# Performance work log

Hardware: AMD Instinct MI355X
Metric: run time of the kernel (lower is better)

## Reference

```python
import jax, jax.numpy as jnp
import numpy as np

C = 256
G = 32            # GroupNorm groups = min(32, C)
DQK = C // 8      # q/k channel dim
EPS = 1e-5


def setup_inputs() -> dict:
    key = jax.random.key(0)
    ks = jax.random.split(key, 10)
    B, H, W = 4, 64, 64
    s = 0.02
    return {
        "x": jax.random.normal(ks[0], (B, C, H, W), dtype=jnp.float32),
        "gamma": jnp.ones((C,), jnp.float32),
        "beta": jnp.zeros((C,), jnp.float32),
        "wq": jax.random.normal(ks[1], (DQK, C), jnp.float32) * s,
        "bq": jnp.zeros((DQK,), jnp.float32),
        "wk": jax.random.normal(ks[2], (DQK, C), jnp.float32) * s,
        "bk": jnp.zeros((DQK,), jnp.float32),
        "wv": jax.random.normal(ks[3], (C, C), jnp.float32) * s,
        "bv": jnp.zeros((C,), jnp.float32),
        "wp": jax.random.normal(ks[4], (C, C), jnp.float32) * s,
        "bp": jnpp if False else jnp.zeros((C,), jnp.float32),
    }


def reference(x, gamma, beta, wq, bq, wk, bk, wv, bv, wp, bp):
    B, Cc, H, W = x.shape
    N = H * W
    # GroupNorm(32, C), affine
    h = x.reshape(B, G, Cc // G, H, W)
    mu = h.mean(axis=(2, 3, 4), keepdims=True)
    var = h.var(axis=(2, 3, 4), keepdims=True)
    h = (h - mu) * jax.lax.rsqrt(var + EPS)
    h = h.reshape(B, Cc, N) * gamma[:, None] + beta[:, None]
    # 1x1 convs == per-token linear maps over channels
    q = jnp.einsum('dc,bcn->bnd', wq, h) + bq            # [B, N, DQK]
    k = jnp.einsum('dc,bcn->bdn', wk, h) + bk[:, None]   # [B, DQK, N]
    v = jnp.einsum('ec,bcn->ben', wv, h) + bv[:, None]   # [B, C, N]
    scale = DQK ** (-0.5)
    attn = jax.nn.softmax(jnp.einsum('bnd,bdm->bnm', q, k) * scale, axis=-1)
    out = jnp.einsum('bnm,bem->ben', attn, v)            # [B, C, N]
    proj = jnp.einsum('fe,ben->bfn', wp, out) + bp[:, None]
    return x + proj.reshape(B, Cc, H, W)
```

## Files before the change

### kernel.cpp

```cpp
#include <hip/hip_runtime.h>
#include <hip/hip_bf16.h>

#define NB 4
#define CD 256
#define NT 4096
#define DQ 32

typedef __attribute__((ext_vector_type(8))) __bf16 bf16x8;
typedef __attribute__((ext_vector_type(4))) float float4v;
typedef __attribute__((ext_vector_type(16))) float float16v;
typedef __attribute__((ext_vector_type(4))) unsigned int uint4v;
typedef __attribute__((ext_vector_type(2))) unsigned int uint2v;

#if __has_builtin(__builtin_amdgcn_exp2f)
#define EXP2(x) __builtin_amdgcn_exp2f(x)
#else
#define EXP2(x) exp2f(x)
#endif

__device__ inline unsigned short f2bf(float f) {
  unsigned u = __float_as_uint(f);
  u += 0x7fffu + ((u >> 16) & 1u);
  return (unsigned short)(u >> 16);
}

__global__ __launch_bounds__(256) void gn_prep(
    const float* __restrict__ x, float* __restrict__ accum,
    const float* __restrict__ wq, const float* __restrict__ wk,
    const float* __restrict__ wv, const float* __restrict__ wp,
    const float* __restrict__ bq, const float* __restrict__ bk,
    const float* __restrict__ bv, unsigned short* __restrict__ wqkv,
    unsigned short* __restrict__ wpb, float* __restrict__ bias) {
  int bx = blockIdx.x;
  int tid = threadIdx.x;
  if (bx < 512) {
    int bg = bx >> 2, ch = bx & 3;
    const float4* xp = (const float4*)(x + (size_t)bg * 32768 + ch * 8192);
    float s = 0.f, ss = 0.f;
#pragma unroll
    for (int i = 0; i < 8; i++) {
      float4 v = xp[tid + 256 * i];
      s += v.x + v.y + v.z + v.w;
      ss += v.x * v.x + v.y * v.y + v.z * v.z + v.w * v.w;
    }
    int wid = tid >> 6, lane = tid & 63;
#pragma unroll
    for (int off = 32; off >= 1; off >>= 1) {
      s += __shfl_xor(s, off);
      ss += __shfl_xor(ss, off);
    }
    __shared__ float red[8];
    if (lane == 0) { red[wid] = s; red[4 + wid] = ss; }
    __syncthreads();
    if (tid == 0) {
      accum[2 * bx] = red[0] + red[1] + red[2] + red[3];
      accum[2 * bx + 1] = red[4] + red[5] + red[6] + red[7];
    }
  } else {
    const float scale2 = 0.2550348909867343f;
    int i = (bx - 512) * 256 + tid;
    if (i < 320 * 256) {
      int j = i >> 8, c = i & 255;
      float v;
      if (j < 32) v = wq[j * 256 + c] * scale2;
      else if (j < 64) v = wk[(j - 32) * 256 + c];
      else v = wv[(j - 64) * 256 + c];
      wqkv[i] = f2bf(v);
    } else if (i < 320 * 256 + 256 * 256) {
      int k = i - 320 * 256;
      wpb[k] = f2bf(wp[k]);
    } else if (i < 320 * 256 + 256 * 256 + 320) {
      int j = i - (320 * 256 + 256 * 256);
      float v;
      if (j < 32) v = bq[j] * scale2;
      else if (j < 64) v = bk[j - 32];
      else v = bv[j - 64];
      bias[j] = v;
    }
  }
}

__global__ __launch_bounds__(256) void gn_apply(
    const float* __restrict__ x, const float* __restrict__ gamma,
    const float* __restrict__ beta, const float* __restrict__ accum,
    unsigned short* __restrict__ h) {
  int bg = blockIdx.x >> 2, nc = blockIdx.x & 3;
  int tid = threadIdx.x;
  float S = accum[8 * bg] + accum[8 * bg + 2] + accum[8 * bg + 4] +
            accum[8 * bg + 6];
  float SS = accum[8 * bg + 1] + accum[8 * bg + 3] + accum[8 * bg + 5] +
             accum[8 * bg + 7];
  float mu = S * (1.f / 32768.f);
  float var = SS * (1.f / 32768.f) - mu * mu;
  float rstd = rsqrtf(var + 1e-5f);
  int b = bg >> 5, g = bg & 31, c0 = g * 8;
  float gam[8], bet[8];
#pragma unroll
  for (int j = 0; j < 8; j++) { gam[j] = gamma[c0 + j]; bet[j] = beta[c0 + j]; }
  const float* xb = x + (size_t)bg * 32768;
#pragma unroll
  for (int i = 0; i < 4; i++) {
    int n = nc * 1024 + tid + 256 * i;
    unsigned short hv[8];
#pragma unroll
    for (int j = 0; j < 8; j++) {
      float y = (xb[j * NT + n] - mu) * rstd * gam[j] + bet[j];
      hv[j] = f2bf(y);
    }
    *(uint4v*)(h + ((size_t)(b * NT + n) * CD + c0)) = *(uint4v*)hv;
  }
}

__global__ __launch_bounds__(256) void qkv_gemm(
    const unsigned short* __restrict__ A, const unsigned short* __restrict__ H,
    const float* __restrict__ bias, unsigned short* __restrict__ qk,
    unsigned short* __restrict__ v) {
  int nt = blockIdx.x, mt = blockIdx.y, b = blockIdx.z;
  int tid = threadIdx.x, lane = tid & 63;
  int w = tid >> 6, mi = w & 1, ni = w >> 1;
  int l31 = lane & 31, hh = lane >> 5;
  int m_base = mt * 64 + 32 * mi;
  int n_base = nt * 128 + 64 * ni;
  const unsigned short* Arow = A + (size_t)(m_base + l31) * 256 + 8 * hh;
  const unsigned short* Hb = H + (size_t)b * NT * CD;
  const unsigned short* h0 = Hb + (size_t)(n_base + l31) * CD + 8 * hh;
  const unsigned short* h1 = h0 + (size_t)32 * CD;
  float16v acc0, acc1;
#pragma unroll
  for (int r = 0; r < 16; r++) { acc0[r] = 0.f; acc1[r] = 0.f; }
#pragma unroll
  for (int s = 0; s < 16; s++) {
    bf16x8 af = *(const bf16x8*)(Arow + 16 * s);
    bf16x8 b0 = *(const bf16x8*)(h0 + 16 * s);
    bf16x8 b1 = *(const bf16x8*)(h1 + 16 * s);
    acc0 = __builtin_amdgcn_mfma_f32_32x32x16_bf16(af, b0, acc0, 0, 0, 0);
    acc1 = __builtin_amdgcn_mfma_f32_32x32x16_bf16(af, b1, acc1, 0, 0, 0);
  }
  float bj[16];
  int jr[16];
#pragma unroll
  for (int r = 0; r < 16; r++) {
    jr[r] = m_base + (r & 3) + 8 * (r >> 2) + 4 * hh;
    bj[r] = bias[jr[r]];
  }
#pragma unroll
  for (int half = 0; half < 2; half++) {
    int n = n_base + 32 * half + l31;
#pragma unroll
    for (int r = 0; r < 16; r++) {
      float val = (half ? acc1[r] : acc0[r]) + bj[r];
      int j = jr[r];
      if (j < 64) {
        qk[((size_t)b * NT + n) * 64 + j] = f2bf(val);
      } else {
        v[((size_t)b * CD + (j - 64)) * NT + n] = f2bf(val);
      }
    }
  }
}

__global__ __launch_bounds__(256) void attn_fused(
    const unsigned short* __restrict__ qk, const unsigned short* __restrict__ V,
    unsigned short* __restrict__ Pa, unsigned short* __restrict__ Pb,
    float* __restrict__ lp4) {
  int bx = blockIdx.x;
  int n0 = (bx >> 1) * 64;
  int kh = bx & 1;
  int E0 = blockIdx.y * 128;
  int b = blockIdx.z;
  int tid = threadIdx.x, lane = tid & 63, w = tid >> 6;
  int qi = w & 1, ei = w >> 1;
  int l31 = lane & 31, hh = lane >> 5;

  __shared__ unsigned short Ks[64 * 36];
  __shared__ unsigned short Vs[128 * 68];
  __shared__ unsigned short Pbuf[2 * 32 * 68];

  const unsigned short* qkb = qk + (size_t)b * NT * 64;
  const unsigned short* Vb = V + (size_t)b * CD * NT;

  int n_g = n0 + 32 * qi + l31;
  bf16x8 qfr[2];
  qfr[0] = *(const bf16x8*)&qkb[(size_t)n_g * 64 + 8 * hh];
  qfr[1] = *(const bf16x8*)&qkb[(size_t)n_g * 64 + 8 * hh + 16];

  int se = tid >> 1, smh = (tid & 1) * 32;
  int skr = tid >> 2, skc = (tid & 3) * 8;

  int mbase = kh * 2048;
  uint4v vreg[4];
  uint4v kreg;
  {
    const unsigned short* vp = &Vb[(size_t)(E0 + se) * NT + mbase + smh];
#pragma unroll
    for (int u = 0; u < 4; u++) vreg[u] = *(const uint4v*)(vp + 8 * u);
    kreg = *(const uint4v*)&qkb[(size_t)(mbase + skr) * 64 + 32 + skc];
  }

  float16v acc[2];
#pragma unroll
  for (int et = 0; et < 2; et++)
#pragma unroll
    for (int r = 0; r < 16; r++) acc[et][r] = 0.f;
  float lsum = 0.f;
  unsigned short* Prow = &Pbuf[(qi * 32 + l31) * 68];

  for (int it = 0; it < 32; it++) {
    *(uint4v*)&Ks[skr * 36 + skc] = kreg;
    if (it + 1 < 32) {
      int m1 = mbase + (it + 1) * 64;
      kreg = *(const uint4v*)&qkb[(size_t)(m1 + skr) * 64 + 32 + skc];
    }
    __syncthreads();

#pragma unroll
    for (int u = 0; u < 4; u++)
      *(uint4v*)&Vs[se * 68 + smh + 8 * u] = vreg[u];
    if (it + 1 < 32) {
      int m1 = mbase + (it + 1) * 64;
      const unsigned short* vp = &Vb[(size_t)(E0 + se) * NT + m1 + smh];
#pragma unroll
      for (int u = 0; u < 4; u++) vreg[u] = *(const uint4v*)(vp + 8 * u);
    }

    float16v st;
#pragma unroll
    for (int r = 0; r < 16; r++) st[r] = 0.f;
#pragma unroll
    for (int s = 0; s < 2; s++) {
      bf16x8 af = *(const bf16x8*)&Ks[(32 * ei + l31) * 36 + 16 * s + 8 * hh];
      st = __builtin_amdgcn_mfma_f32_32x32x16_bf16(af, qfr[s], st, 0, 0, 0);
    }
#pragma unroll
    for (int rq = 0; rq < 4; rq++) {
      float e0 = EXP2(st[4 * rq + 0]);
      float e1 = EXP2(st[4 * rq + 1]);
      float e2 = EXP2(st[4 * rq + 2]);
      float e3 = EXP2(st[4 * rq + 3]);
      lsum += (e0 + e1) + (e2 + e3);
      uint2v pw;
      pw[0] = __builtin_amdgcn_perm(__float_as_uint(e1), __float_as_uint(e0),
                                    0x07060302u);
      pw[1] = __builtin_amdgcn_perm(__float_as_uint(e3), __float_as_uint(e2),
                                    0x07060302u);
      *(uint2v*)&Prow[8 * rq + 4 * hh + 32 * ei] = pw;
    }
    __syncthreads();

#pragma unroll
    for (int sp = 0; sp < 4; sp++) {
      bf16x8 afr =
          *(const bf16x8*)&Pbuf[(qi * 32 + l31) * 68 + 16 * sp + 8 * hh];
#pragma unroll
      for (int et = 0; et < 2; et++) {
        bf16x8 bfr = *(const bf16x8*)&Vs[(64 * ei + 32 * et + l31) * 68 +
                                         16 * sp + 8 * hh];
        acc[et] =
            __builtin_amdgcn_mfma_f32_32x32x16_bf16(afr, bfr, acc[et], 0, 0, 0);
      }
    }
  }

  lsum += __shfl_xor(lsum, 32);
  unsigned short* Pout = (kh ? Pb : Pa) + (size_t)b * NT * CD;
#pragma unroll
  for (int r = 0; r < 16; r++) {
    int nl = (r & 3) + 8 * (r >> 2) + 4 * hh;
    size_t row = (size_t)(n0 + 32 * qi + nl) * CD + E0 + 64 * ei + l31;
#pragma unroll
    for (int et = 0; et < 2; et++) {
      Pout[row + 32 * et] = f2bf(acc[et][r]);
    }
  }
  if (hh == 0) {
    lp4[(size_t)((kh * 2 + ei) * NB + b) * NT + n0 + 32 * qi + l31] = lsum;
  }
}

__device__ inline bf16x8 combine_frag(const unsigned short* p0,
                                      const unsigned short* p1, float inv) {
  uint4v ua = *(const uint4v*)p0;
  uint4v ub = *(const uint4v*)p1;
  uint4v r;
#pragma unroll
  for (int j = 0; j < 4; j++) {
    float lo = __uint_as_float(ua[j] << 16) + __uint_as_float(ub[j] << 16);
    float hi = __uint_as_float(ua[j] & 0xffff0000u) +
               __uint_as_float(ub[j] & 0xffff0000u);
    lo *= inv;
    hi *= inv;
    r[j] = __builtin_amdgcn_perm(__float_as_uint(hi), __float_as_uint(lo),
                                 0x07060302u);
  }
  return *(bf16x8*)&r;
}

__global__ __launch_bounds__(256) void proj_gemm(
    const unsigned short* __restrict__ Wp, const unsigned short* __restrict__ Pa,
    const unsigned short* __restrict__ Pb, const float* __restrict__ lp4,
    const float* __restrict__ bp, const float* __restrict__ x,
    float* __restrict__ out) {
  int nt = blockIdx.x, mt = blockIdx.y, b = blockIdx.z;
  int tid = threadIdx.x, lane = tid & 63;
  int w = tid >> 6, mi = w & 1, ni = w >> 1;
  int l31 = lane & 31, hh = lane >> 5;
  int m_base = mt * 64 + 32 * mi;
  int n_base = nt * 128 + 64 * ni;
  const unsigned short* Arow = Wp + (size_t)(m_base + l31) * 256 + 8 * hh;
  int nA = n_base + l31, nB = nA + 32;
  float lA = 0.f, lB = 0.f;
#pragma unroll
  for (int s4 = 0; s4 < 4; s4++) {
    lA += lp4[(size_t)(s4 * NB + b) * NT + nA];
    lB += lp4[(size_t)(s4 * NB + b) * NT + nB];
  }
  float invA = 1.f / lA, invB = 1.f / lB;
  const unsigned short* a0 = Pa + ((size_t)b * NT + nA) * CD + 8 * hh;
  const unsigned short* a1 = Pa + ((size_t)b * NT + nB) * CD + 8 * hh;
  const unsigned short* c0 = Pb + ((size_t)b * NT + nA) * CD + 8 * hh;
  const unsigned short* c1 = Pb + ((size_t)b * NT + nB) * CD + 8 * hh;
  float16v acc0, acc1;
#pragma unroll
  for (int r = 0; r < 16; r++) { acc0[r] = 0.f; acc1[r] = 0.f; }
#pragma unroll
  for (int s = 0; s < 16; s++) {
    bf16x8 af = *(const bf16x8*)(Arow + 16 * s);
    bf16x8 b0 = combine_frag(a0 + 16 * s, c0 + 16 * s, invA);
    bf16x8 b1 = combine_frag(a1 + 16 * s, c1 + 16 * s, invB);
    acc0 = __builtin_amdgcn_mfma_f32_32x32x16_bf16(af, b0, acc0, 0, 0, 0);
    acc1 = __builtin_amdgcn_mfma_f32_32x32x16_bf16(af, b1, acc1, 0, 0, 0);
  }
#pragma unroll
  for (int half = 0; half < 2; half++) {
    int n = n_base + 32 * half + l31;
#pragma unroll
    for (int r = 0; r < 16; r++) {
      int f = m_base + (r & 3) + 8 * (r >> 2) + 4 * hh;
      size_t idx = ((size_t)b * CD + f) * NT + n;
      out[idx] = x[idx] + (half ? acc1[r] : acc0[r]) + bp[f];
    }
  }
}

extern "C" void kernel_launch(void* const* d_in, const int* in_sizes, int n_in,
                              void* d_out, int out_size, void* d_ws,
                              size_t ws_size, hipStream_t stream) {
  (void)in_sizes; (void)n_in; (void)out_size; (void)ws_size;
  const float* x = (const float*)d_in[0];
  const float* gamma = (const float*)d_in[1];
  const float* beta = (const float*)d_in[2];
  const float* wq = (const float*)d_in[3];
  const float* bq = (const float*)d_in[4];
  const float* wk = (const float*)d_in[5];
  const float* bk = (const float*)d_in[6];
  const float* wv = (const float*)d_in[7];
  const float* bv = (const float*)d_in[8];
  const float* wp = (const float*)d_in[9];
  const float* bp = (const float*)d_in[10];
  float* out = (float*)d_out;

  char* ws = (char*)d_ws;
  unsigned short* h_ws = (unsigned short*)ws;
  unsigned short* qk_ws = (unsigned short*)(ws + 8388608);
  unsigned short* v_ws = (unsigned short*)(ws + 10485760);
  unsigned short* o_ws = (unsigned short*)(ws + 18874368);
  unsigned short* wqkv_b = (unsigned short*)(ws + 27262976);
  unsigned short* wp_b = (unsigned short*)(ws + 27426816);
  float* bias_q = (float*)(ws + 27557888);
  float* accum = (float*)(ws + 27559168);
  float* lp4 = (float*)(ws + 27563264);

  gn_prep<<<1090, 256, 0, stream>>>(x, accum, wq, wk, wv, wp, bq, bk, bv,
                                    wqkv_b, wp_b, bias_q);
  gn_apply<<<512, 256, 0, stream>>>(x, gamma, beta, accum, h_ws);
  dim3 gq(32, 5, NB);
  qkv_gemm<<<gq, 256, 0, stream>>>(wqkv_b, h_ws, bias_q, qk_ws, v_ws);
  dim3 ga(128, 2, NB);
  attn_fused<<<ga, 256, 0, stream>>>(qk_ws, v_ws, h_ws, o_ws, lp4);
  dim3 gp(32, 4, NB);
  proj_gemm<<<gp, 256, 0, stream>>>(wp_b, h_ws, o_ws, lp4, bp, x, out);
}
```

Before: 207.9 us.

## Merge five kernels into one cooperative persistent kernel with grid syncs

Replaces the five separate launches (stats/weight prep, groupnorm apply, QKV GEMM, attention, projection) with a single cooperative kernel of 512 persistent blocks. The blocks loop over each stage's work items and separate the stages with grid-wide barriers. The aim is to remove per-launch overhead and the gaps between kernels. In exchange, the stages with 640 and 1024 work items no longer divide evenly across 512 blocks, grid syncs have their own cost, and occupancy is capped by the launch bounds and shared-memory use.

```diff
diff --git a/kernel.cpp b/kernel.cpp
--- a/kernel.cpp
+++ b/kernel.cpp
@@ -1,13 +1,15 @@
 #include <hip/hip_runtime.h>
 #include <hip/hip_bf16.h>
+#include <hip/hip_cooperative_groups.h>
 
 #define NB 4
 #define CD 256
 #define NT 4096
 #define DQ 32
 
+namespace cg = cooperative_groups;
+
 typedef __attribute__((ext_vector_type(8))) __bf16 bf16x8;
-typedef __attribute__((ext_vector_type(4))) float float4v;
 typedef __attribute__((ext_vector_type(16))) float float16v;
 typedef __attribute__((ext_vector_type(4))) unsigned int uint4v;
 typedef __attribute__((ext_vector_type(2))) unsigned int uint2v;
@@ -22,259 +24,6 @@
   unsigned u = __float_as_uint(f);
   u += 0x7fffu + ((u >> 16) & 1u);
   return (unsigned short)(u >> 16);
-}
-
-__global__ __launch_bounds__(256) void gn_prep(
-    const float* __restrict__ x, float* __restrict__ accum,
-    const float* __restrict__ wq, const float* __restrict__ wk,
-    const float* __restrict__ wv, const float* __restrict__ wp,
-    const float* __restrict__ bq, const float* __restrict__ bk,
-    const float* __restrict__ bv, unsigned short* __restrict__ wqkv,
-    unsigned short* __restrict__ wpb, float* __restrict__ bias) {
-  int bx = blockIdx.x;
-  int tid = threadIdx.x;
-  if (bx < 512) {
-    int bg = bx >> 2, ch = bx & 3;
-    const float4* xp = (const float4*)(x + (size_t)bg * 32768 + ch * 8192);
-    float s = 0.f, ss = 0.f;
-#pragma unroll
-    for (int i = 0; i < 8; i++) {
-      float4 v = xp[tid + 256 * i];
-      s += v.x + v.y + v.z + v.w;
-      ss += v.x * v.x + v.y * v.y + v.z * v.z + v.w * v.w;
-    }
-    int wid = tid >> 6, lane = tid & 63;
-#pragma unroll
-    for (int off = 32; off >= 1; off >>= 1) {
-      s += __shfl_xor(s, off);
-      ss += __shfl_xor(ss, off);
-    }
-    __shared__ float red[8];
-    if (lane == 0) { red[wid] = s; red[4 + wid] = ss; }
-    __syncthreads();
-    if (tid == 0) {
-      accum[2 * bx] = red[0] + red[1] + red[2] + red[3];
-      accum[2 * bx + 1] = red[4] + red[5] + red[6] + red[7];
-    }
-  } else {
-    const float scale2 = 0.2550348909867343f;
-    int i = (bx - 512) * 256 + tid;
-    if (i < 320 * 256) {
-      int j = i >> 8, c = i & 255;
-      float v;
-      if (j < 32) v = wq[j * 256 + c] * scale2;
-      else if (j < 64) v = wk[(j - 32) * 256 + c];
-      else v = wv[(j - 64) * 256 + c];
-      wqkv[i] = f2bf(v);
-    } else if (i < 320 * 256 + 256 * 256) {
-      int k = i - 320 * 256;
-      wpb[k] = f2bf(wp[k]);
-    } else if (i < 320 * 256 + 256 * 256 + 320) {
-      int j = i - (320 * 256 + 256 * 256);
-      float v;
-      if (j < 32) v = bq[j] * scale2;
-      else if (j < 64) v = bk[j - 32];
-      else v = bv[j - 64];
-      bias[j] = v;
-    }
-  }
-}
-
-__global__ __launch_bounds__(256) void gn_apply(
-    const float* __restrict__ x, const float* __restrict__ gamma,
-    const float* __restrict__ beta, const float* __restrict__ accum,
-    unsigned short* __restrict__ h) {
-  int bg = blockIdx.x >> 2, nc = blockIdx.x & 3;
-  int tid = threadIdx.x;
-  float S = accum[8 * bg] + accum[8 * bg + 2] + accum[8 * bg + 4] +
-            accum[8 * bg + 6];
-  float SS = accum[8 * bg + 1] + accum[8 * bg + 3] + accum[8 * bg + 5] +
-             accum[8 * bg + 7];
-  float mu = S * (1.f / 32768.f);
-  float var = SS * (1.f / 32768.f) - mu * mu;
-  float rstd = rsqrtf(var + 1e-5f);
-  int b = bg >> 5, g = bg & 31, c0 = g * 8;
-  float gam[8], bet[8];
-#pragma unroll
-  for (int j = 0; j < 8; j++) { gam[j] = gamma[c0 + j]; bet[j] = beta[c0 + j]; }
-  const float* xb = x + (size_t)bg * 32768;
-#pragma unroll
-  for (int i = 0; i < 4; i++) {
-    int n = nc * 1024 + tid + 256 * i;
-    unsigned short hv[8];
-#pragma unroll
-    for (int j = 0; j < 8; j++) {
-      float y = (xb[j * NT + n] - mu) * rstd * gam[j] + bet[j];
-      hv[j] = f2bf(y);
-    }
-    *(uint4v*)(h + ((size_t)(b * NT + n) * CD + c0)) = *(uint4v*)hv;
-  }
-}
-
-__global__ __launch_bounds__(256) void qkv_gemm(
-    const unsigned short* __restrict__ A, const unsigned short* __restrict__ H,
-    const float* __restrict__ bias, unsigned short* __restrict__ qk,
-    unsigned short* __restrict__ v) {
-  int nt = blockIdx.x, mt = blockIdx.y, b = blockIdx.z;
-  int tid = threadIdx.x, lane = tid & 63;
-  int w = tid >> 6, mi = w & 1, ni = w >> 1;
-  int l31 = lane & 31, hh = lane >> 5;
-  int m_base = mt * 64 + 32 * mi;
-  int n_base = nt * 128 + 64 * ni;
-  const unsigned short* Arow = A + (size_t)(m_base + l31) * 256 + 8 * hh;
-  const unsigned short* Hb = H + (size_t)b * NT * CD;
-  const unsigned short* h0 = Hb + (size_t)(n_base + l31) * CD + 8 * hh;
-  const unsigned short* h1 = h0 + (size_t)32 * CD;
-  float16v acc0, acc1;
-#pragma unroll
-  for (int r = 0; r < 16; r++) { acc0[r] = 0.f; acc1[r] = 0.f; }
-#pragma unroll
-  for (int s = 0; s < 16; s++) {
-    bf16x8 af = *(const bf16x8*)(Arow + 16 * s);
-    bf16x8 b0 = *(const bf16x8*)(h0 + 16 * s);
-    bf16x8 b1 = *(const bf16x8*)(h1 + 16 * s);
-    acc0 = __builtin_amdgcn_mfma_f32_32x32x16_bf16(af, b0, acc0, 0, 0, 0);
-    acc1 = __builtin_amdgcn_mfma_f32_32x32x16_bf16(af, b1, acc1, 0, 0, 0);
-  }
-  float bj[16];
-  int jr[16];
-#pragma unroll
-  for (int r = 0; r < 16; r++) {
-    jr[r] = m_base + (r & 3) + 8 * (r >> 2) + 4 * hh;
-    bj[r] = bias[jr[r]];
-  }
-#pragma unroll
-  for (int half = 0; half < 2; half++) {
-    int n = n_base + 32 * half + l31;
-#pragma unroll
-    for (int r = 0; r < 16; r++) {
-      float val = (half ? acc1[r] : acc0[r]) + bj[r];
-      int j = jr[r];
-      if (j < 64) {
-        qk[((size_t)b * NT + n) * 64 + j] = f2bf(val);
-      } else {
-        v[((size_t)b * CD + (j - 64)) * NT + n] = f2bf(val);
-      }
-    }
-  }
-}
-
-__global__ __launch_bounds__(256) void attn_fused(
-    const unsigned short* __restrict__ qk, const unsigned short* __restrict__ V,
-    unsigned short* __restrict__ Pa, unsigned short* __restrict__ Pb,
-    float* __restrict__ lp4) {
-  int bx = blockIdx.x;
-  int n0 = (bx >> 1) * 64;
-  int kh = bx & 1;
-  int E0 = blockIdx.y * 128;
-  int b = blockIdx.z;
-  int tid = threadIdx.x, lane = tid & 63, w = tid >> 6;
-  int qi = w & 1, ei = w >> 1;
-  int l31 = lane & 31, hh = lane >> 5;
-
-  __shared__ unsigned short Ks[64 * 36];
-  __shared__ unsigned short Vs[128 * 68];
-  __shared__ unsigned short Pbuf[2 * 32 * 68];
-
-  const unsigned short* qkb = qk + (size_t)b * NT * 64;
-  const unsigned short* Vb = V + (size_t)b * CD * NT;
-
-  int n_g = n0 + 32 * qi + l31;
-  bf16x8 qfr[2];
-  qfr[0] = *(const bf16x8*)&qkb[(size_t)n_g * 64 + 8 * hh];
-  qfr[1] = *(const bf16x8*)&qkb[(size_t)n_g * 64 + 8 * hh + 16];
-
-  int se = tid >> 1, smh = (tid & 1) * 32;
-  int skr = tid >> 2, skc = (tid & 3) * 8;
-
-  int mbase = kh * 2048;
-  uint4v vreg[4];
-  uint4v kreg;
-  {
-    const unsigned short* vp = &Vb[(size_t)(E0 + se) * NT + mbase + smh];
-#pragma unroll
-    for (int u = 0; u < 4; u++) vreg[u] = *(const uint4v*)(vp + 8 * u);
-    kreg = *(const uint4v*)&qkb[(size_t)(mbase + skr) * 64 + 32 + skc];
-  }
-
-  float16v acc[2];
-#pragma unroll
-  for (int et = 0; et < 2; et++)
-#pragma unroll
-    for (int r = 0; r < 16; r++) acc[et][r] = 0.f;
-  float lsum = 0.f;
-  unsigned short* Prow = &Pbuf[(qi * 32 + l31) * 68];
-
-  for (int it = 0; it < 32; it++) {
-    *(uint4v*)&Ks[skr * 36 + skc] = kreg;
-    if (it + 1 < 32) {
-      int m1 = mbase + (it + 1) * 64;
-      kreg = *(const uint4v*)&qkb[(size_t)(m1 + skr) * 64 + 32 + skc];
-    }
-    __syncthreads();
-
-#pragma unroll
-    for (int u = 0; u < 4; u++)
-      *(uint4v*)&Vs[se * 68 + smh + 8 * u] = vreg[u];
-    if (it + 1 < 32) {
-      int m1 = mbase + (it + 1) * 64;
-      const unsigned short* vp = &Vb[(size_t)(E0 + se) * NT + m1 + smh];
-#pragma unroll
-      for (int u = 0; u < 4; u++) vreg[u] = *(const uint4v*)(vp + 8 * u);
-    }
-
-    float16v st;
-#pragma unroll
-    for (int r = 0; r < 16; r++) st[r] = 0.f;
-#pragma unroll
-    for (int s = 0; s < 2; s++) {
-      bf16x8 af = *(const bf16x8*)&Ks[(32 * ei + l31) * 36 + 16 * s + 8 * hh];
-      st = __builtin_amdgcn_mfma_f32_32x32x16_bf16(af, qfr[s], st, 0, 0, 0);
-    }
-#pragma unroll
-    for (int rq = 0; rq < 4; rq++) {
-      float e0 = EXP2(st[4 * rq + 0]);
-      float e1 = EXP2(st[4 * rq + 1]);
-      float e2 = EXP2(st[4 * rq + 2]);
-      float e3 = EXP2(st[4 * rq + 3]);
-      lsum += (e0 + e1) + (e2 + e3);
-      uint2v pw;
-      pw[0] = __builtin_amdgcn_perm(__float_as_uint(e1), __float_as_uint(e0),
-                                    0x07060302u);
-      pw[1] = __builtin_amdgcn_perm(__float_as_uint(e3), __float_as_uint(e2),
-                                    0x07060302u);
-      *(uint2v*)&Prow[8 * rq + 4 * hh + 32 * ei] = pw;
-    }
-    __syncthreads();
-
-#pragma unroll
-    for (int sp = 0; sp < 4; sp++) {
-      bf16x8 afr =
-          *(const bf16x8*)&Pbuf[(qi * 32 + l31) * 68 + 16 * sp + 8 * hh];
-#pragma unroll
-      for (int et = 0; et < 2; et++) {
-        bf16x8 bfr = *(const bf16x8*)&Vs[(64 * ei + 32 * et + l31) * 68 +
-                                         16 * sp + 8 * hh];
-        acc[et] =
-            __builtin_amdgcn_mfma_f32_32x32x16_bf16(afr, bfr, acc[et], 0, 0, 0);
-      }
-    }
-  }
-
-  lsum += __shfl_xor(lsum, 32);
-  unsigned short* Pout = (kh ? Pb : Pa) + (size_t)b * NT * CD;
-#pragma unroll
-  for (int r = 0; r < 16; r++) {
-    int nl = (r & 3) + 8 * (r >> 2) + 4 * hh;
-    size_t row = (size_t)(n0 + 32 * qi + nl) * CD + E0 + 64 * ei + l31;
-#pragma unroll
-    for (int et = 0; et < 2; et++) {
-      Pout[row + 32 * et] = f2bf(acc[et][r]);
-    }
-  }
-  if (hh == 0) {
-    lp4[(size_t)((kh * 2 + ei) * NB + b) * NT + n0 + 32 * qi + l31] = lsum;
-  }
 }
 
 __device__ inline bf16x8 combine_frag(const unsigned short* p0,
@@ -295,49 +44,320 @@
   return *(bf16x8*)&r;
 }
 
-__global__ __launch_bounds__(256) void proj_gemm(
-    const unsigned short* __restrict__ Wp, const unsigned short* __restrict__ Pa,
-    const unsigned short* __restrict__ Pb, const float* __restrict__ lp4,
-    const float* __restrict__ bp, const float* __restrict__ x,
-    float* __restrict__ out) {
-  int nt = blockIdx.x, mt = blockIdx.y, b = blockIdx.z;
-  int tid = threadIdx.x, lane = tid & 63;
-  int w = tid >> 6, mi = w & 1, ni = w >> 1;
-  int l31 = lane & 31, hh = lane >> 5;
-  int m_base = mt * 64 + 32 * mi;
-  int n_base = nt * 128 + 64 * ni;
-  const unsigned short* Arow = Wp + (size_t)(m_base + l31) * 256 + 8 * hh;
-  int nA = n_base + l31, nB = nA + 32;
-  float lA = 0.f, lB = 0.f;
-#pragma unroll
-  for (int s4 = 0; s4 < 4; s4++) {
-    lA += lp4[(size_t)(s4 * NB + b) * NT + nA];
-    lB += lp4[(size_t)(s4 * NB + b) * NT + nB];
-  }
-  float invA = 1.f / lA, invB = 1.f / lB;
-  const unsigned short* a0 = Pa + ((size_t)b * NT + nA) * CD + 8 * hh;
-  const unsigned short* a1 = Pa + ((size_t)b * NT + nB) * CD + 8 * hh;
-  const unsigned short* c0 = Pb + ((size_t)b * NT + nA) * CD + 8 * hh;
-  const unsigned short* c1 = Pb + ((size_t)b * NT + nB) * CD + 8 * hh;
-  float16v acc0, acc1;
-#pragma unroll
-  for (int r = 0; r < 16; r++) { acc0[r] = 0.f; acc1[r] = 0.f; }
-#pragma unroll
-  for (int s = 0; s < 16; s++) {
-    bf16x8 af = *(const bf16x8*)(Arow + 16 * s);
-    bf16x8 b0 = combine_frag(a0 + 16 * s, c0 + 16 * s, invA);
-    bf16x8 b1 = combine_frag(a1 + 16 * s, c1 + 16 * s, invB);
-    acc0 = __builtin_amdgcn_mfma_f32_32x32x16_bf16(af, b0, acc0, 0, 0, 0);
-    acc1 = __builtin_amdgcn_mfma_f32_32x32x16_bf16(af, b1, acc1, 0, 0, 0);
-  }
-#pragma unroll
-  for (int half = 0; half < 2; half++) {
-    int n = n_base + 32 * half + l31;
+__global__ __launch_bounds__(256, 2) void fused_all(
+    const float* __restrict__ x, const float* __restrict__ gamma,
+    const float* __restrict__ beta, const float* __restrict__ wq,
+    const float* __restrict__ bq, const float* __restrict__ wk,
+    const float* __restrict__ bk, const float* __restrict__ wv,
+    const float* __restrict__ bv, const float* __restrict__ wp,
+    const float* __restrict__ bp, float* __restrict__ out,
+    char* __restrict__ ws) {
+  cg::grid_group grid = cg::this_grid();
+  int tid = threadIdx.x;
+  int nblk = (int)gridDim.x;
+
+  unsigned short* Pa = (unsigned short*)ws;
+  unsigned short* qk = (unsigned short*)(ws + 8388608);
+  unsigned short* v = (unsigned short*)(ws + 10485760);
+  unsigned short* Pb = (unsigned short*)(ws + 18874368);
+  unsigned short* wqkv = (unsigned short*)(ws + 27262976);
+  unsigned short* wpb = (unsigned short*)(ws + 27426816);
+  float* bias = (float*)(ws + 27557888);
+  float* accum = (float*)(ws + 27559168);
+  float* lp4 = (float*)(ws + 27563264);
+  unsigned short* h = Pa;
+
+  __shared__ alignas(16) char smem_raw[30720];
+
+  for (int u = blockIdx.x; u < 1090; u += nblk) {
+    __syncthreads();
+    if (u < 512) {
+      int bg = u >> 2, ch = u & 3;
+      const float4* xp = (const float4*)(x + (size_t)bg * 32768 + ch * 8192);
+      float s = 0.f, ss = 0.f;
+#pragma unroll
+      for (int i = 0; i < 8; i++) {
+        float4 vv = xp[tid + 256 * i];
+        s += vv.x + vv.y + vv.z + vv.w;
+        ss += vv.x * vv.x + vv.y * vv.y + vv.z * vv.z + vv.w * vv.w;
+      }
+      int wid = tid >> 6, lane = tid & 63;
+#pragma unroll
+      for (int off = 32; off >= 1; off >>= 1) {
+        s += __shfl_xor(s, off);
+        ss += __shfl_xor(ss, off);
+      }
+      float* red = (float*)smem_raw;
+      if (lane == 0) { red[wid] = s; red[4 + wid] = ss; }
+      __syncthreads();
+      if (tid == 0) {
+        accum[2 * u] = red[0] + red[1] + red[2] + red[3];
+        accum[2 * u + 1] = red[4] + red[5] + red[6] + red[7];
+      }
+    } else {
+      const float scale2 = 0.2550348909867343f;
+      int i = (u - 512) * 256 + tid;
+      if (i < 320 * 256) {
+        int j = i >> 8, c = i & 255;
+        float vv;
+        if (j < 32) vv = wq[j * 256 + c] * scale2;
+        else if (j < 64) vv = wk[(j - 32) * 256 + c];
+        else vv = wv[(j - 64) * 256 + c];
+        wqkv[i] = f2bf(vv);
+      } else if (i < 320 * 256 + 256 * 256) {
+        int k = i - 320 * 256;
+        wpb[k] = f2bf(wp[k]);
+      } else if (i < 320 * 256 + 256 * 256 + 320) {
+        int j = i - (320 * 256 + 256 * 256);
+        float vv;
+        if (j < 32) vv = bq[j] * scale2;
+        else if (j < 64) vv = bk[j - 32];
+        else vv = bv[j - 64];
+        bias[j] = vv;
+      }
+    }
+  }
+  grid.sync();
+
+  for (int u = blockIdx.x; u < 512; u += nblk) {
+    int bg = u >> 2, nc = u & 3;
+    float S = accum[8 * bg] + accum[8 * bg + 2] + accum[8 * bg + 4] +
+              accum[8 * bg + 6];
+    float SS = accum[8 * bg + 1] + accum[8 * bg + 3] + accum[8 * bg + 5] +
+               accum[8 * bg + 7];
+    float mu = S * (1.f / 32768.f);
+    float var = SS * (1.f / 32768.f) - mu * mu;
+    float rstd = rsqrtf(var + 1e-5f);
+    int b = bg >> 5, g = bg & 31, c0 = g * 8;
+    float gam[8], bet[8];
+#pragma unroll
+    for (int j = 0; j < 8; j++) {
+      gam[j] = gamma[c0 + j];
+      bet[j] = beta[c0 + j];
+    }
+    const float* xb = x + (size_t)bg * 32768;
+#pragma unroll
+    for (int i = 0; i < 4; i++) {
+      int n = nc * 1024 + tid + 256 * i;
+      unsigned short hv[8];
+#pragma unroll
+      for (int j = 0; j < 8; j++) {
+        float y = (xb[j * NT + n] - mu) * rstd * gam[j] + bet[j];
+        hv[j] = f2bf(y);
+      }
+      *(uint4v*)(h + ((size_t)(b * NT + n) * CD + c0)) = *(uint4v*)hv;
+    }
+  }
+  grid.sync();
+
+  for (int u = blockIdx.x; u < 640; u += nblk) {
+    int b = u / 160;
+    int rem = u - 160 * b;
+    int mt = rem >> 5, nt = rem & 31;
+    int lane = tid & 63;
+    int w = tid >> 6, mi = w & 1, ni = w >> 1;
+    int l31 = lane & 31, hh = lane >> 5;
+    int m_base = mt * 64 + 32 * mi;
+    int n_base = nt * 128 + 64 * ni;
+    const unsigned short* Arow = wqkv + (size_t)(m_base + l31) * 256 + 8 * hh;
+    const unsigned short* Hb = h + (size_t)b * NT * CD;
+    const unsigned short* h0 = Hb + (size_t)(n_base + l31) * CD + 8 * hh;
+    const unsigned short* h1 = h0 + (size_t)32 * CD;
+    float16v acc0, acc1;
+#pragma unroll
+    for (int r = 0; r < 16; r++) { acc0[r] = 0.f; acc1[r] = 0.f; }
+#pragma unroll
+    for (int s = 0; s < 16; s++) {
+      bf16x8 af = *(const bf16x8*)(Arow + 16 * s);
+      bf16x8 b0 = *(const bf16x8*)(h0 + 16 * s);
+      bf16x8 b1 = *(const bf16x8*)(h1 + 16 * s);
+      acc0 = __builtin_amdgcn_mfma_f32_32x32x16_bf16(af, b0, acc0, 0, 0, 0);
+      acc1 = __builtin_amdgcn_mfma_f32_32x32x16_bf16(af, b1, acc1, 0, 0, 0);
+    }
+    float bj[16];
+    int jr[16];
 #pragma unroll
     for (int r = 0; r < 16; r++) {
-      int f = m_base + (r & 3) + 8 * (r >> 2) + 4 * hh;
-      size_t idx = ((size_t)b * CD + f) * NT + n;
-      out[idx] = x[idx] + (half ? acc1[r] : acc0[r]) + bp[f];
+      jr[r] = m_base + (r & 3) + 8 * (r >> 2) + 4 * hh;
+      bj[r] = bias[jr[r]];
+    }
+#pragma unroll
+    for (int half = 0; half < 2; half++) {
+      int n = n_base + 32 * half + l31;
+#pragma unroll
+      for (int r = 0; r < 16; r++) {
+        float val = (half ? acc1[r] : acc0[r]) + bj[r];
+        int j = jr[r];
+        if (j < 64) {
+          qk[((size_t)b * NT + n) * 64 + j] = f2bf(val);
+        } else {
+          v[((size_t)b * CD + (j - 64)) * NT + n] = f2bf(val);
+        }
+      }
+    }
+  }
+  grid.sync();
+
+  {
+    unsigned short* Ks = (unsigned short*)smem_raw;
+    unsigned short* Vs = Ks + 64 * 36;
+    unsigned short* Pbuf = Vs + 128 * 68;
+    for (int u = blockIdx.x; u < 1024; u += nblk) {
+      int bx = u & 127;
+      int E0 = ((u >> 7) & 1) * 128;
+      int b = u >> 8;
+      int n0 = (bx >> 1) * 64;
+      int kh = bx & 1;
+      int lane = tid & 63, w = tid >> 6;
+      int qi = w & 1, ei = w >> 1;
+      int l31 = lane & 31, hh = lane >> 5;
+
+      const unsigned short* qkb = qk + (size_t)b * NT * 64;
+      const unsigned short* Vb = v + (size_t)b * CD * NT;
+
+      int n_g = n0 + 32 * qi + l31;
+      bf16x8 qfr[2];
+      qfr[0] = *(const bf16x8*)&qkb[(size_t)n_g * 64 + 8 * hh];
+      qfr[1] = *(const bf16x8*)&qkb[(size_t)n_g * 64 + 8 * hh + 16];
+
+      int se = tid >> 1, smh = (tid & 1) * 32;
+      int skr = tid >> 2, skc = (tid & 3) * 8;
+
+      int mbase = kh * 2048;
+      uint4v vreg[4];
+      uint4v kreg;
+      {
+        const unsigned short* vp = &Vb[(size_t)(E0 + se) * NT + mbase + smh];
+#pragma unroll
+        for (int uu = 0; uu < 4; uu++) vreg[uu] = *(const uint4v*)(vp + 8 * uu);
+        kreg = *(const uint4v*)&qkb[(size_t)(mbase + skr) * 64 + 32 + skc];
+      }
+
+      float16v acc[2];
+#pragma unroll
+      for (int et = 0; et < 2; et++)
+#pragma unroll
+        for (int r = 0; r < 16; r++) acc[et][r] = 0.f;
+      float lsum = 0.f;
+      unsigned short* Prow = &Pbuf[(qi * 32 + l31) * 68];
+
+      __syncthreads();
+      for (int it = 0; it < 32; it++) {
+        *(uint4v*)&Ks[skr * 36 + skc] = kreg;
+        if (it + 1 < 32) {
+          int m1 = mbase + (it + 1) * 64;
+          kreg = *(const uint4v*)&qkb[(size_t)(m1 + skr) * 64 + 32 + skc];
+        }
+        __syncthreads();
+
+#pragma unroll
+        for (int uu = 0; uu < 4; uu++)
+          *(uint4v*)&Vs[se * 68 + smh + 8 * uu] = vreg[uu];
+        if (it + 1 < 32) {
+          int m1 = mbase + (it + 1) * 64;
+          const unsigned short* vp = &Vb[(size_t)(E0 + se) * NT + m1 + smh];
+#pragma unroll
+          for (int uu = 0; uu < 4; uu++)
+            vreg[uu] = *(const uint4v*)(vp + 8 * uu);
+        }
+
+        float16v st;
+#pragma unroll
+        for (int r = 0; r < 16; r++) st[r] = 0.f;
+#pragma unroll
+        for (int s = 0; s < 2; s++) {
+          bf16x8 af =
+              *(const bf16x8*)&Ks[(32 * ei + l31) * 36 + 16 * s + 8 * hh];
+          st = __builtin_amdgcn_mfma_f32_32x32x16_bf16(af, qfr[s], st, 0, 0, 0);
+        }
+#pragma unroll
+        for (int rq = 0; rq < 4; rq++) {
+          float e0 = EXP2(st[4 * rq + 0]);
+          float e1 = EXP2(st[4 * rq + 1]);
+          float e2 = EXP2(st[4 * rq + 2]);
+          float e3 = EXP2(st[4 * rq + 3]);
+          lsum += (e0 + e1) + (e2 + e3);
+          uint2v pw;
+          pw[0] = __builtin_amdgcn_perm(__float_as_uint(e1),
+                                        __float_as_uint(e0), 0x07060302u);
+          pw[1] = __builtin_amdgcn_perm(__float_as_uint(e3),
+                                        __float_as_uint(e2), 0x07060302u);
+          *(uint2v*)&Prow[8 * rq + 4 * hh + 32 * ei] = pw;
+        }
+        __syncthreads();
+
+#pragma unroll
+        for (int sp = 0; sp < 4; sp++) {
+          bf16x8 afr =
+              *(const bf16x8*)&Pbuf[(qi * 32 + l31) * 68 + 16 * sp + 8 * hh];
+#pragma unroll
+          for (int et = 0; et < 2; et++) {
+            bf16x8 bfr = *(const bf16x8*)&Vs[(64 * ei + 32 * et + l31) * 68 +
+                                             16 * sp + 8 * hh];
+            acc[et] = __builtin_amdgcn_mfma_f32_32x32x16_bf16(afr, bfr, acc[et],
+                                                              0, 0, 0);
+          }
+        }
+      }
+
+      lsum += __shfl_xor(lsum, 32);
+      unsigned short* Pout = (kh ? Pb : Pa) + (size_t)b * NT * CD;
+#pragma unroll
+      for (int r = 0; r < 16; r++) {
+        int nl = (r & 3) + 8 * (r >> 2) + 4 * hh;
+        size_t row = (size_t)(n0 + 32 * qi + nl) * CD + E0 + 64 * ei + l31;
+#pragma unroll
+        for (int et = 0; et < 2; et++) {
+          Pout[row + 32 * et] = f2bf(acc[et][r]);
+        }
+      }
+      if (hh == 0) {
+        lp4[(size_t)((kh * 2 + ei) * NB + b) * NT + n0 + 32 * qi + l31] = lsum;
+      }
+    }
+  }
+  grid.sync();
+
+  for (int u = blockIdx.x; u < 512; u += nblk) {
+    int nt = u & 31, mt = (u >> 5) & 3, b = u >> 7;
+    int lane = tid & 63;
+    int w = tid >> 6, mi = w & 1, ni = w >> 1;
+    int l31 = lane & 31, hh = lane >> 5;
+    int m_base = mt * 64 + 32 * mi;
+    int n_base = nt * 128 + 64 * ni;
+    const unsigned short* Arow = wpb + (size_t)(m_base + l31) * 256 + 8 * hh;
+    int nA = n_base + l31, nB = nA + 32;
+    float lA = 0.f, lB = 0.f;
+#pragma unroll
+    for (int s4 = 0; s4 < 4; s4++) {
+      lA += lp4[(size_t)(s4 * NB + b) * NT + nA];
+      lB += lp4[(size_t)(s4 * NB + b) * NT + nB];
+    }
+    float invA = 1.f / lA, invB = 1.f / lB;
+    const unsigned short* a0 = Pa + ((size_t)b * NT + nA) * CD + 8 * hh;
+    const unsigned short* a1 = Pa + ((size_t)b * NT + nB) * CD + 8 * hh;
+    const unsigned short* c0 = Pb + ((size_t)b * NT + nA) * CD + 8 * hh;
+    const unsigned short* c1 = Pb + ((size_t)b * NT + nB) * CD + 8 * hh;
+    float16v acc0, acc1;
+#pragma unroll
+    for (int r = 0; r < 16; r++) { acc0[r] = 0.f; acc1[r] = 0.f; }
+#pragma unroll
+    for (int s = 0; s < 16; s++) {
+      bf16x8 af = *(const bf16x8*)(Arow + 16 * s);
+      bf16x8 b0 = combine_frag(a0 + 16 * s, c0 + 16 * s, invA);
+      bf16x8 b1 = combine_frag(a1 + 16 * s, c1 + 16 * s, invB);
+      acc0 = __builtin_amdgcn_mfma_f32_32x32x16_bf16(af, b0, acc0, 0, 0, 0);
+      acc1 = __builtin_amdgcn_mfma_f32_32x32x16_bf16(af, b1, acc1, 0, 0, 0);
+    }
+#pragma unroll
+    for (int half = 0; half < 2; half++) {
+      int n = n_base + 32 * half + l31;
+#pragma unroll
+      for (int r = 0; r < 16; r++) {
+        int f = m_base + (r & 3) + 8 * (r >> 2) + 4 * hh;
+        size_t idx = ((size_t)b * CD + f) * NT + n;
+        out[idx] = x[idx] + (half ? acc1[r] : acc0[r]) + bp[f];
+      }
     }
   }
 }
@@ -358,25 +378,12 @@
   const float* wp = (const float*)d_in[9];
   const float* bp = (const float*)d_in[10];
   float* out = (float*)d_out;
-
   char* ws = (char*)d_ws;
-  unsigned short* h_ws = (unsigned short*)ws;
-  unsigned short* qk_ws = (unsigned short*)(ws + 8388608);
-  unsigned short* v_ws = (unsigned short*)(ws + 10485760);
-  unsigned short* o_ws = (unsigned short*)(ws + 18874368);
-  unsigned short* wqkv_b = (unsigned short*)(ws + 27262976);
-  unsigned short* wp_b = (unsigned short*)(ws + 27426816);
-  float* bias_q = (float*)(ws + 27557888);
-  float* accum = (float*)(ws + 27559168);
-  float* lp4 = (float*)(ws + 27563264);
-
-  gn_prep<<<1090, 256, 0, stream>>>(x, accum, wq, wk, wv, wp, bq, bk, bv,
-                                    wqkv_b, wp_b, bias_q);
-  gn_apply<<<512, 256, 0, stream>>>(x, gamma, beta, accum, h_ws);
-  dim3 gq(32, 5, NB);
-  qkv_gemm<<<gq, 256, 0, stream>>>(wqkv_b, h_ws, bias_q, qk_ws, v_ws);
-  dim3 ga(128, 2, NB);
-  attn_fused<<<ga, 256, 0, stream>>>(qk_ws, v_ws, h_ws, o_ws, lp4);
-  dim3 gp(32, 4, NB);
-  proj_gemm<<<gp, 256, 0, stream>>>(wp_b, h_ws, o_ws, lp4, bp, x, out);
+
+  void* args[] = {(void*)&x,  (void*)&gamma, (void*)&beta, (void*)&wq,
+                  (void*)&bq, (void*)&wk,    (void*)&bk,   (void*)&wv,
+                  (void*)&bv, (void*)&wp,    (void*)&bp,   (void*)&out,
+                  (void*)&ws};
+  hipLaunchCooperativeKernel((const void*)fused_all, dim3(512), dim3(256),
+                             args, 0, stream);
 }
```

After: 685.8 us. +229.9%, slower.

## Merge both channel halves into one 512-thread attention block to share softmax work

Applied to the files above, without the earlier changes.

The attention kernel previously ran two blocks per query tile, one for each 128-channel half of V, and each recomputed QK^T scores and exponentials. Now a single 512-thread block covers all 256 channels. Only half the waves compute the scores and write P to shared memory, and all eight waves then do the PV MFMAs from a doubled V tile in LDS. This removes the duplicated QK and exp work and the duplicate K loads. In exchange the grid has half as many blocks, LDS use per block is larger, and half the waves sit idle during the score phase.

```diff
diff --git a/kernel.cpp b/kernel.cpp
--- a/kernel.cpp
+++ b/kernel.cpp
@@ -7,7 +7,6 @@
 #define DQ 32
 
 typedef __attribute__((ext_vector_type(8))) __bf16 bf16x8;
-typedef __attribute__((ext_vector_type(4))) float float4v;
 typedef __attribute__((ext_vector_type(16))) float float16v;
 typedef __attribute__((ext_vector_type(4))) unsigned int uint4v;
 typedef __attribute__((ext_vector_type(2))) unsigned int uint2v;
@@ -159,21 +158,20 @@
   }
 }
 
-__global__ __launch_bounds__(256) void attn_fused(
+__global__ __launch_bounds__(512, 4) void attn_fused(
     const unsigned short* __restrict__ qk, const unsigned short* __restrict__ V,
     unsigned short* __restrict__ Pa, unsigned short* __restrict__ Pb,
     float* __restrict__ lp4) {
   int bx = blockIdx.x;
   int n0 = (bx >> 1) * 64;
   int kh = bx & 1;
-  int E0 = blockIdx.y * 128;
-  int b = blockIdx.z;
+  int b = blockIdx.y;
   int tid = threadIdx.x, lane = tid & 63, w = tid >> 6;
-  int qi = w & 1, ei = w >> 1;
+  int qi = w & 1, kj = (w >> 1) & 1, eo = w >> 2;
   int l31 = lane & 31, hh = lane >> 5;
 
   __shared__ unsigned short Ks[64 * 36];
-  __shared__ unsigned short Vs[128 * 68];
+  __shared__ unsigned short Vs[256 * 68];
   __shared__ unsigned short Pbuf[2 * 32 * 68];
 
   const unsigned short* qkb = qk + (size_t)b * NT * 64;
@@ -191,10 +189,11 @@
   uint4v vreg[4];
   uint4v kreg;
   {
-    const unsigned short* vp = &Vb[(size_t)(E0 + se) * NT + mbase + smh];
+    const unsigned short* vp = &Vb[(size_t)se * NT + mbase + smh];
 #pragma unroll
     for (int u = 0; u < 4; u++) vreg[u] = *(const uint4v*)(vp + 8 * u);
-    kreg = *(const uint4v*)&qkb[(size_t)(mbase + skr) * 64 + 32 + skc];
+    if (tid < 256)
+      kreg = *(const uint4v*)&qkb[(size_t)(mbase + skr) * 64 + 32 + skc];
   }
 
   float16v acc[2];
@@ -206,10 +205,12 @@
   unsigned short* Prow = &Pbuf[(qi * 32 + l31) * 68];
 
   for (int it = 0; it < 32; it++) {
-    *(uint4v*)&Ks[skr * 36 + skc] = kreg;
-    if (it + 1 < 32) {
-      int m1 = mbase + (it + 1) * 64;
-      kreg = *(const uint4v*)&qkb[(size_t)(m1 + skr) * 64 + 32 + skc];
+    if (tid < 256) {
+      *(uint4v*)&Ks[skr * 36 + skc] = kreg;
+      if (it + 1 < 32) {
+        int m1 = mbase + (it + 1) * 64;
+        kreg = *(const uint4v*)&qkb[(size_t)(m1 + skr) * 64 + 32 + skc];
+      }
     }
     __syncthreads();
 
@@ -218,32 +219,34 @@
       *(uint4v*)&Vs[se * 68 + smh + 8 * u] = vreg[u];
     if (it + 1 < 32) {
       int m1 = mbase + (it + 1) * 64;
-      const unsigned short* vp = &Vb[(size_t)(E0 + se) * NT + m1 + smh];
+      const unsigned short* vp = &Vb[(size_t)se * NT + m1 + smh];
 #pragma unroll
       for (int u = 0; u < 4; u++) vreg[u] = *(const uint4v*)(vp + 8 * u);
     }
 
-    float16v st;
-#pragma unroll
-    for (int r = 0; r < 16; r++) st[r] = 0.f;
-#pragma unroll
-    for (int s = 0; s < 2; s++) {
-      bf16x8 af = *(const bf16x8*)&Ks[(32 * ei + l31) * 36 + 16 * s + 8 * hh];
-      st = __builtin_amdgcn_mfma_f32_32x32x16_bf16(af, qfr[s], st, 0, 0, 0);
-    }
-#pragma unroll
-    for (int rq = 0; rq < 4; rq++) {
-      float e0 = EXP2(st[4 * rq + 0]);
-      float e1 = EXP2(st[4 * rq + 1]);
-      float e2 = EXP2(st[4 * rq + 2]);
-      float e3 = EXP2(st[4 * rq + 3]);
-      lsum += (e0 + e1) + (e2 + e3);
-      uint2v pw;
-      pw[0] = __builtin_amdgcn_perm(__float_as_uint(e1), __float_as_uint(e0),
-                                    0x07060302u);
-      pw[1] = __builtin_amdgcn_perm(__float_as_uint(e3), __float_as_uint(e2),
-                                    0x07060302u);
-      *(uint2v*)&Prow[8 * rq + 4 * hh + 32 * ei] = pw;
+    if (eo == 0) {
+      float16v st;
+#pragma unroll
+      for (int r = 0; r < 16; r++) st[r] = 0.f;
+#pragma unroll
+      for (int s = 0; s < 2; s++) {
+        bf16x8 af = *(const bf16x8*)&Ks[(32 * kj + l31) * 36 + 16 * s + 8 * hh];
+        st = __builtin_amdgcn_mfma_f32_32x32x16_bf16(af, qfr[s], st, 0, 0, 0);
+      }
+#pragma unroll
+      for (int rq = 0; rq < 4; rq++) {
+        float e0 = EXP2(st[4 * rq + 0]);
+        float e1 = EXP2(st[4 * rq + 1]);
+        float e2 = EXP2(st[4 * rq + 2]);
+        float e3 = EXP2(st[4 * rq + 3]);
+        lsum += (e0 + e1) + (e2 + e3);
+        uint2v pw;
+        pw[0] = __builtin_amdgcn_perm(__float_as_uint(e1), __float_as_uint(e0),
+                                      0x07060302u);
+        pw[1] = __builtin_amdgcn_perm(__float_as_uint(e3), __float_as_uint(e2),
+                                      0x07060302u);
+        *(uint2v*)&Prow[8 * rq + 4 * hh + 32 * kj] = pw;
+      }
     }
     __syncthreads();
 
@@ -253,27 +256,31 @@
           *(const bf16x8*)&Pbuf[(qi * 32 + l31) * 68 + 16 * sp + 8 * hh];
 #pragma unroll
       for (int et = 0; et < 2; et++) {
-        bf16x8 bfr = *(const bf16x8*)&Vs[(64 * ei + 32 * et + l31) * 68 +
-                                         16 * sp + 8 * hh];
+        int etile = 4 * eo + 2 * kj + et;
+        bf16x8 bfr =
+            *(const bf16x8*)&Vs[(32 * etile + l31) * 68 + 16 * sp + 8 * hh];
         acc[et] =
             __builtin_amdgcn_mfma_f32_32x32x16_bf16(afr, bfr, acc[et], 0, 0, 0);
       }
     }
   }
 
-  lsum += __shfl_xor(lsum, 32);
+  if (eo == 0) {
+    lsum += __shfl_xor(lsum, 32);
+    if (hh == 0) {
+      lp4[(size_t)((kh * 2 + kj) * NB + b) * NT + n0 + 32 * qi + l31] = lsum;
+    }
+  }
   unsigned short* Pout = (kh ? Pb : Pa) + (size_t)b * NT * CD;
 #pragma unroll
   for (int r = 0; r < 16; r++) {
     int nl = (r & 3) + 8 * (r >> 2) + 4 * hh;
-    size_t row = (size_t)(n0 + 32 * qi + nl) * CD + E0 + 64 * ei + l31;
+    size_t row = (size_t)(n0 + 32 * qi + nl) * CD + l31;
 #pragma unroll
     for (int et = 0; et < 2; et++) {
-      Pout[row + 32 * et] = f2bf(acc[et][r]);
-    }
-  }
-  if (hh == 0) {
-    lp4[(size_t)((kh * 2 + ei) * NB + b) * NT + n0 + 32 * qi + l31] = lsum;
+      int etile = 4 * eo + 2 * kj + et;
+      Pout[row + 32 * etile] = f2bf(acc[et][r]);
+    }
   }
 }
 
@@ -375,8 +382,8 @@
   gn_apply<<<512, 256, 0, stream>>>(x, gamma, beta, accum, h_ws);
   dim3 gq(32, 5, NB);
   qkv_gemm<<<gq, 256, 0, stream>>>(wqkv_b, h_ws, bias_q, qk_ws, v_ws);
-  dim3 ga(128, 2, NB);
-  attn_fused<<<ga, 256, 0, stream>>>(qk_ws, v_ws, h_ws, o_ws, lp4);
+  dim3 ga(128, NB);
+  attn_fused<<<ga, 512, 0, stream>>>(qk_ws, v_ws, h_ws, o_ws, lp4);
   dim3 gp(32, 4, NB);
   proj_gemm<<<gp, 256, 0, stream>>>(wp_b, h_ws, o_ws, lp4, bp, x, out);
 }
```

New measurement: 192.4 us. -7.4%, faster.
